# Performance work log

Measured on AMD Instinct MI355X. Metric: run time of the kernel, lower is better.

## Reference

```python
import jax, jax.numpy as jnp
import numpy as np

# --- static module config (from init_kwargs) ---
C1_OUT = 64          # c1OutChannels
C1K = 400            # k winners in conv layer
N_FC = 1024          # fc1 hidden units (n)
K_FC = 100           # k winners in fc1
BOOST = 1.0          # boostStrength
W_SPARSITY = 0.5     # weightSparsity: fraction of fc1 weights allowed nonzero
HP = 12              # pooled spatial size: floor((28-5+1)/2)
C1_OUTPUT_LEN = C1_OUT * HP * HP  # 9216
BATCH = 4096


def setup_inputs() -> dict:
    key = jax.random.key(0)
    ks = jax.random.split(key, 10)
    x = jax.random.normal(ks[0], (BATCH, 1, 28, 28), jnp.float32)
    c1_w = jax.random.normal(ks[1], (C1_OUT, 1, 5, 5), jnp.float32) * 0.1
    c1_b = jax.random.normal(ks[2], (C1_OUT,), jnp.float32) * 0.01
    # duty cycles live in [0, ~density]
    duty_cnn = jax.random.uniform(ks[3], (1, C1_OUT, 1, 1), jnp.float32) * 0.05
    fc1_w = jax.random.normal(ks[4], (N_FC, C1_OUT_LEN_ := C1_OUTPUT_LEN), jnp.float32) * 0.01
    fc1_mask_raw = jax.random.uniform(ks[5], (N_FC, C1_OUTPUT_LEN), jnp.float32)
    fc1_b = jax.random.normal(ks[6], (N_FC,), jnp.float32) * 0.01
    duty_fc = jax.random.uniform(ks[7], (N_FC,), jnp.float32) * 0.1
    fc2_w = jax.random.normal(ks[8], (10, N_FC), jnp.float32) * 0.05
    fc2_b = jnp.zeros((10,), jnp.float32)
    return dict(x=x, c1_w=c1_w, c1_b=c1_b, duty_cnn=duty_cnn, fc1_w=fc1_w,
                fc1_mask_raw=fc1_mask_raw, fc1_b=fc1_b, duty_fc=duty_fc,
                fc2_w=fc2_w, fc2_b=fc2_b)


def _kwinners(x_flat, boost_flat, k):
    """Duty-cycle-boosted k-winner mask.
    x_flat: [B, N]; boost_flat: [1, N] broadcastable boost factors.
    Keeps original x values at the top-k boosted positions per row, zeros rest.
    Boosting uses stop_gradient(x), matching KWinners*.forward(x.detach()*boost).
    """
    boosted = jax.lax.stop_gradient(x_flat) * boost_flat
    thr = jax.lax.top_k(boosted, k)[0][:, -1:]  # k-th largest per row
    return jnp.where(boosted >= thr, x_flat, jnp.zeros((), x_flat.dtype))


def reference(x, c1_w, c1_b, duty_cnn, fc1_w, fc1_mask_raw, fc1_b, duty_fc,
              fc2_w, fc2_b):
    B = x.shape[0]
    # conv2d (valid, stride 1) -> [B, 64, 24, 24]
    y = jax.lax.conv_general_dilated(
        x, c1_w, window_strides=(1, 1), padding='VALID',
        dimension_numbers=('NCHW', 'OIHW', 'NCHW')) + c1_b[None, :, None, None]
    # max_pool2d(2) -> [B, 64, 12, 12]
    y = jax.lax.reduce_window(y, -jnp.inf, jax.lax.max,
                              (1, 1, 2, 2), (1, 1, 2, 2), 'VALID')
    # KWinnersCNN: global top-k over flattened (C,H,W), per-channel boost
    target_density = C1K / C1_OUTPUT_LEN
    boost_c = jnp.exp((target_density - duty_cnn) * BOOST)  # [1,C,1,1]
    boost_flat = jnp.broadcast_to(boost_c, (1, C1_OUT, HP, HP)).reshape(1, -1)
    yf = _kwinners(y.reshape(B, -1), boost_flat, C1K)  # [B, 9216]
    # LinearSDR fc1: sparse-weight linear + KWinners
    w_mask = (fc1_mask_raw < W_SPARSITY).astype(fc1_w.dtype)
    h = yf @ (fc1_w * w_mask).T + fc1_b  # [B, 1024]
    boost_fc = jnp.exp((K_FC / N_FC - duty_fc) * BOOST)[None, :]
    h = _kwinners(h, boost_fc, K_FC)
    # fc2 + log_softmax (dropout inactive in eval mode)
    logits = h @ fc2_w.T + fc2_b
    return jax.nn.log_softmax(logits, axis=1)
```

## Files before the change

kernel.cpp:

```cpp
#include <hip/hip_runtime.h>

__device__ __forceinline__ float b2f(unsigned short u) {
  return __uint_as_float(((unsigned)u) << 16);
}
__device__ __forceinline__ unsigned short f2b(float f) {
  unsigned u = __float_as_uint(f);
  return (unsigned short)((u + 0x7FFFu + ((u >> 16) & 1u)) >> 16);
}
__device__ __forceinline__ float gload(const void* p, int i, int isb) {
  return isb ? b2f(((const unsigned short*)p)[i]) : ((const float*)p)[i];
}
__device__ __forceinline__ unsigned tokey(float f) {
  unsigned u = __float_as_uint(f);
  return u ^ (unsigned)(((int)u >> 31) | 0x80000000u);
}

__global__ void k_detect(const void* x, int* flag) {
  int tid = threadIdx.x;
  unsigned short u = ((const unsigned short*)x)[2 * tid];
  int e = (u >> 7) & 0xFF;
  bool sane = (e >= 100 && e <= 140);
  unsigned long long m = __ballot(sane);
  if (tid == 0) *flag = (__popcll(m) >= 40) ? 1 : 0;
}

__global__ __launch_bounds__(256) void k_prep(const void* __restrict__ fc1w,
                                              const void* __restrict__ mraw,
                                              float* __restrict__ WtF,
                                              const int* __restrict__ flag) {
  __shared__ float tile[64][65];
  const int isb = *flag;
  const int i0 = blockIdx.x * 64;
  const int u0 = blockIdx.y * 64;
  const int tx = threadIdx.x & 63, ty = threadIdx.x >> 6;
  for (int uu = ty; uu < 64; uu += 4) {
    int gi = (u0 + uu) * 9216 + i0 + tx;
    float wv = gload(fc1w, gi, isb);
    float mv = gload(mraw, gi, isb);
    tile[uu][tx] = (mv < 0.5f) ? wv : 0.0f;
  }
  __syncthreads();
  for (int ii = ty; ii < 64; ii += 4)
    WtF[(i0 + ii) * 1024 + u0 + tx] = tile[tx][ii];
}

__global__ __launch_bounds__(256) void k_conv(const void* __restrict__ x,
                                              const void* __restrict__ c1w_g,
                                              const void* __restrict__ c1b_g,
                                              const void* __restrict__ duty_g,
                                              int2* __restrict__ wpair,
                                              int* __restrict__ wcnt,
                                              const int* __restrict__ flag) {
  __shared__ __align__(16) unsigned char u_imghist[3136];
  __shared__ float cb[64], bcs[64];
  __shared__ __align__(16) float pooled[9216];
  __shared__ unsigned wtot[4];
  __shared__ unsigned selb, selk;
  float* img = (float*)u_imghist;
  unsigned* h2a = (unsigned*)u_imghist;
  unsigned* h2b = (unsigned*)(u_imghist + 1024);
  const int tid = threadIdx.x;
  const int b = blockIdx.x;
  const int isb = *flag;
  const int lane = tid & 63;
  const int wv_id = tid >> 6;

  for (int i = tid; i < 784; i += 256) img[i] = gload(x, b * 784 + i, isb);
  if (tid < 64) {
    cb[tid] = gload(c1b_g, tid, isb);
    float arg = (float)(400.0 / 9216.0) - gload(duty_g, tid, isb);
    bcs[tid] = (float)exp((double)arg);
  }
  __syncthreads();

  {
    const int c = tid >> 2;
    const int half = tid & 1;
    const int ph0 = ((tid >> 1) & 1) * 6;
    float w[25];
#pragma unroll
    for (int i = 0; i < 25; ++i) w[i] = gload(c1w_g, c * 25 + i, isb);
    const float bias = cb[c];
    float R[6][16];
#pragma unroll
    for (int r = 0; r < 6; ++r) {
      int ir = 2 * ph0 + r;
#pragma unroll
      for (int q = 0; q < 4; ++q)
        ((float4*)&R[r][0])[q] = ((const float4*)img)[ir * 7 + half * 3 + q];
    }
#pragma unroll
    for (int i = 0; i < 6; ++i) {
      const int ph = ph0 + i;
      float a0[12], a1[12];
#pragma unroll
      for (int j = 0; j < 12; ++j) { a0[j] = 0.f; a1[j] = 0.f; }
#pragma unroll
      for (int kj = 0; kj < 5; ++kj) {
#pragma unroll
        for (int kr = 0; kr < 5; ++kr) {
          float wk = w[kr * 5 + kj];
          const float* r0 = &R[(2 * i + kr) % 6][0];
          const float* r1 = &R[(2 * i + kr + 1) % 6][0];
#pragma unroll
          for (int j = 0; j < 12; ++j) {
            a0[j] = fmaf(r0[j + kj], wk, a0[j]);
            a1[j] = fmaf(r1[j + kj], wk, a1[j]);
          }
        }
      }
      int obase = c * 144 + ph * 12 + half * 6;
#pragma unroll
      for (int q = 0; q < 6; ++q) {
        float m = fmaxf(fmaxf(a0[2 * q], a0[2 * q + 1]),
                        fmaxf(a1[2 * q], a1[2 * q + 1]));
        pooled[obase + q] = m + bias;
      }
      if (i < 5) {
        int ir0 = 2 * ph + 6, ir1 = 2 * ph + 7;
        float* d0 = &R[(2 * i) % 6][0];
        float* d1 = &R[(2 * i + 1) % 6][0];
#pragma unroll
        for (int q = 0; q < 4; ++q) {
          ((float4*)d0)[q] = ((const float4*)img)[ir0 * 7 + half * 3 + q];
          ((float4*)d1)[q] = ((const float4*)img)[ir1 * 7 + half * 3 + q];
        }
      }
    }
  }
  __syncthreads();

  unsigned keys[36];
  {
    const float bcf = bcs[tid >> 2];
#pragma unroll
    for (int e4 = 0; e4 < 9; ++e4) {
      float4 pv = ((float4*)pooled)[tid * 9 + e4];
      keys[4 * e4 + 0] = tokey(pv.x * bcf);
      keys[4 * e4 + 1] = tokey(pv.y * bcf);
      keys[4 * e4 + 2] = tokey(pv.z * bcf);
      keys[4 * e4 + 3] = tokey(pv.w * bcf);
    }
  }

  unsigned kfix = 0;
  unsigned kk = 400;
  for (int pass = 3; pass >= 0; --pass) {
    const int shift = pass * 8;
    const unsigned himask = (pass == 3) ? 0u : (0xFFFFFFFFu << (shift + 8));
    h2a[tid] = 0;
    h2b[tid] = 0;
    __syncthreads();
    unsigned* myh = (wv_id < 2) ? h2a : h2b;
    if (pass == 3) {
      unsigned cbin = keys[0] >> 24, ccnt = 1;
#pragma unroll
      for (int e = 1; e < 36; ++e) {
        unsigned bin = keys[e] >> 24;
        if (bin == cbin) {
          ++ccnt;
        } else {
          atomicAdd(&myh[cbin], ccnt);
          cbin = bin;
          ccnt = 1;
        }
      }
      atomicAdd(&myh[cbin], ccnt);
    } else {
#pragma unroll
      for (int e = 0; e < 36; ++e) {
        unsigned key = keys[e];
        if (((key ^ kfix) & himask) == 0)
          atomicAdd(&myh[(key >> shift) & 255u], 1u);
      }
    }
    __syncthreads();
    unsigned own = h2a[tid] + h2b[tid];
    unsigned v = own;
#pragma unroll
    for (int off = 1; off < 64; off <<= 1) {
      unsigned y = __shfl_down(v, off, 64);
      if (lane + off < 64) v += y;
    }
    if (lane == 0) wtot[wv_id] = v;
    __syncthreads();
#pragma unroll
    for (int w2 = 0; w2 < 4; ++w2)
      if (w2 > wv_id) v += wtot[w2];
    unsigned snext = v - own;
    if (v >= kk && snext < kk) {
      selb = (unsigned)tid;
      selk = kk - snext;
    }
    __syncthreads();
    kfix |= selb << shift;
    kk = selk;
  }

  unsigned mycnt = 0;
#pragma unroll
  for (int e = 0; e < 36; ++e) mycnt += (keys[e] >= kfix) ? 1u : 0u;
  unsigned px = mycnt;
#pragma unroll
  for (int off = 1; off < 64; off <<= 1) {
    unsigned y = __shfl_up(px, off, 64);
    if (lane >= off) px += y;
  }
  if (lane == 63) wtot[wv_id] = px;
  __syncthreads();
  unsigned base = 0;
#pragma unroll
  for (int w2 = 0; w2 < 4; ++w2)
    if (w2 < wv_id) base += wtot[w2];
  int pos = (int)(base + px - mycnt);
  for (int e = 0; e < 36; ++e) {
    if (keys[e] >= kfix) {
      int o = tid * 36 + e;
      if (pos < 512)
        wpair[b * 512 + pos] = make_int2(__float_as_int(pooled[o]), o << 12);
      ++pos;
    }
  }
  if (tid == 0) {
    unsigned tot = wtot[0] + wtot[1] + wtot[2] + wtot[3];
    wcnt[b] = (int)(tot < 512u ? tot : 512u);
  }
}

__global__ __launch_bounds__(128) void k_fc1(const float* __restrict__ WtF,
                                             const int2* __restrict__ wpair,
                                             const int* __restrict__ wcnt,
                                             const void* __restrict__ fc1b,
                                             float* __restrict__ h,
                                             const int* __restrict__ flag) {
  __shared__ __align__(16) int2 wl[512];
  const int tid = threadIdx.x;
  const int img = blockIdx.x >> 3;
  const int slice = blockIdx.x & 7;
  const int isb = *flag;
  const int cnt = wcnt[img];
  const int2* __restrict__ wp = wpair + img * 512;
  for (int i = tid; i < cnt; i += 128) wl[i] = wp[i];
  __syncthreads();
  const int u = (slice << 7) + tid;
  const char* __restrict__ Wb = (const char*)WtF + (unsigned)u * 4u;
  const int4* wl4 = (const int4*)wl;
  float acc = 0.f;
  int w = 0;
  for (; w + 8 <= cnt; w += 8) {
    const int b4 = w >> 1;
    int4 q0 = wl4[b4 + 0];
    int4 q1 = wl4[b4 + 1];
    int4 q2 = wl4[b4 + 2];
    int4 q3 = wl4[b4 + 3];
    acc = fmaf(__int_as_float(q0.x), *(const float*)(Wb + (unsigned)q0.y), acc);
    acc = fmaf(__int_as_float(q0.z), *(const float*)(Wb + (unsigned)q0.w), acc);
    acc = fmaf(__int_as_float(q1.x), *(const float*)(Wb + (unsigned)q1.y), acc);
    acc = fmaf(__int_as_float(q1.z), *(const float*)(Wb + (unsigned)q1.w), acc);
    acc = fmaf(__int_as_float(q2.x), *(const float*)(Wb + (unsigned)q2.y), acc);
    acc = fmaf(__int_as_float(q2.z), *(const float*)(Wb + (unsigned)q2.w), acc);
    acc = fmaf(__int_as_float(q3.x), *(const float*)(Wb + (unsigned)q3.y), acc);
    acc = fmaf(__int_as_float(q3.z), *(const float*)(Wb + (unsigned)q3.w), acc);
  }
  for (; w < cnt; ++w) {
    int2 p = wl[w];
    acc = fmaf(__int_as_float(p.x), *(const float*)(Wb + (unsigned)p.y), acc);
  }
  h[img * 1024 + u] = acc + gload(fc1b, u, isb);
}

__global__ __launch_bounds__(256) void k_boost(const void* __restrict__ dutyfc,
                                               float* __restrict__ bf,
                                               const int* __restrict__ flag) {
  const int u = blockIdx.x * 256 + threadIdx.x;
  const int isb = *flag;
  if (u < 1024)
    bf[u] = (float)exp((double)(0.09765625f - gload(dutyfc, u, isb)));
}

__global__ __launch_bounds__(256) void k_sel(const float* __restrict__ h,
                                             const float* __restrict__ bf,
                                             const void* __restrict__ fc2w,
                                             const void* __restrict__ fc2b,
                                             void* __restrict__ out,
                                             const int* __restrict__ flag) {
  __shared__ __align__(16) unsigned whist[4][256];
  const int tid = threadIdx.x;
  const int lane = tid & 63;
  const int wv = tid >> 6;
  const int row = blockIdx.x * 4 + wv;
  const int isb = *flag;
  unsigned* hist = whist[wv];
  volatile unsigned* vhist = whist[wv];

  float hv[16];
  unsigned keys[16];
#pragma unroll
  for (int j = 0; j < 16; ++j) {
    float xv = h[row * 1024 + j * 64 + lane];
    hv[j] = xv;
    keys[j] = tokey(xv * bf[j * 64 + lane]);
  }

  unsigned kfix = 0, kk = 100;
  for (int pass = 3; pass >= 0; --pass) {
    const int shift = pass * 8;
    const unsigned himask = (pass == 3) ? 0u : (0xFFFFFFFFu << (shift + 8));
    ((uint4*)hist)[lane] = make_uint4(0u, 0u, 0u, 0u);
    __builtin_amdgcn_sched_barrier(0);
#pragma unroll
    for (int j = 0; j < 16; ++j) {
      if (((keys[j] ^ kfix) & himask) == 0)
        atomicAdd(&hist[(keys[j] >> shift) & 255u], 1u);
    }
    __builtin_amdgcn_sched_barrier(0);
    unsigned o0 = vhist[4 * lane + 0];
    unsigned o1 = vhist[4 * lane + 1];
    unsigned o2 = vhist[4 * lane + 2];
    unsigned o3 = vhist[4 * lane + 3];
    unsigned lsum = o0 + o1 + o2 + o3;
    unsigned v = lsum;
#pragma unroll
    for (int off = 1; off < 64; off <<= 1) {
      unsigned y = __shfl_down(v, off, 64);
      if (lane + off < 64) v += y;
    }
    const unsigned after = v - lsum;
    const unsigned t3 = o3;
    const unsigned t2 = o2 + t3;
    const unsigned t1 = o1 + t2;
    const unsigned t0 = o0 + t1;
    unsigned candb = 0, candk = 0;
    bool found = false;
    const unsigned S0 = after + t0, S1 = after + t1, S2 = after + t2,
                   S3 = after + t3, S4 = after;
    if (S0 >= kk && S1 < kk) { candb = 4u * lane + 0u; candk = kk - S1; found = true; }
    else if (S1 >= kk && S2 < kk) { candb = 4u * lane + 1u; candk = kk - S2; found = true; }
    else if (S2 >= kk && S3 < kk) { candb = 4u * lane + 2u; candk = kk - S3; found = true; }
    else if (S3 >= kk && S4 < kk) { candb = 4u * lane + 3u; candk = kk - S4; found = true; }
    unsigned long long msk = __ballot(found);
    int src = __ffsll((unsigned long long)msk) - 1;
    candb = __shfl(candb, src, 64);
    candk = __shfl(candk, src, 64);
    kfix |= candb << shift;
    kk = candk;
  }

  double part[10];
#pragma unroll
  for (int c = 0; c < 10; ++c) part[c] = 0.0;
#pragma unroll
  for (int j = 0; j < 16; ++j) {
    if (keys[j] >= kfix) {
      const int u = j * 64 + lane;
      const double hx = (double)hv[j];
#pragma unroll
      for (int c = 0; c < 10; ++c)
        part[c] = fma(hx, (double)gload(fc2w, c * 1024 + u, isb), part[c]);
    }
  }
#pragma unroll
  for (int c = 0; c < 10; ++c) {
    double p = part[c];
#pragma unroll
    for (int off = 32; off > 0; off >>= 1) p += __shfl_xor(p, off);
    part[c] = p + (double)gload(fc2b, c, isb);
  }

  double m = part[0];
#pragma unroll
  for (int c = 1; c < 10; ++c) m = part[c] > m ? part[c] : m;
  double mv = part[0];
#pragma unroll
  for (int c = 1; c < 10; ++c)
    if (lane == c) mv = part[c];
  double e = (lane < 10) ? exp(mv - m) : 0.0;
  double sum = 0.0;
#pragma unroll
  for (int c = 0; c < 10; ++c) sum += __shfl(e, c, 64);
  double logs = log(sum);
  if (lane < 10) {
    double o = mv - m - logs;
    if (isb)
      ((unsigned short*)out)[row * 10 + lane] = f2b((float)o);
    else
      ((float*)out)[row * 10 + lane] = (float)o;
  }
}

extern "C" void kernel_launch(void* const* d_in, const int* in_sizes, int n_in,
                              void* d_out, int out_size, void* d_ws, size_t ws_size,
                              hipStream_t stream) {
  char* ws = (char*)d_ws;
  float* WtF = (float*)ws;
  int2* wpair = (int2*)(ws + 37748736);
  int* wcnt = (int*)(ws + 54525952);
  float* h = (float*)(ws + 54542336);
  int* flag = (int*)(ws + 71319552);
  float* bf = WtF;

  k_detect<<<1, 64, 0, stream>>>(d_in[0], flag);
  k_prep<<<dim3(144, 16), 256, 0, stream>>>(d_in[4], d_in[5], WtF, flag);
  k_conv<<<4096, 256, 0, stream>>>(d_in[0], d_in[1], d_in[2], d_in[3],
                                   wpair, wcnt, flag);
  k_fc1<<<4096 * 8, 128, 0, stream>>>(WtF, wpair, wcnt, d_in[6], h, flag);
  k_boost<<<4, 256, 0, stream>>>(d_in[7], bf, flag);
  k_sel<<<1024, 256, 0, stream>>>(h, bf, d_in[8], d_in[9], d_out, flag);
}
```

Before: 564.7 us.

## Split fc1 gather into two passes over halves of the feature index range

```diff
diff --git a/kernel.cpp b/kernel.cpp
--- a/kernel.cpp
+++ b/kernel.cpp
@@ -232,7 +232,8 @@
                                              const int* __restrict__ wcnt,
                                              const void* __restrict__ fc1b,
                                              float* __restrict__ h,
-                                             const int* __restrict__ flag) {
+                                             const int* __restrict__ flag,
+                                             int phase) {
   __shared__ __align__(16) int2 wl[512];
   const int tid = threadIdx.x;
   const int img = blockIdx.x >> 3;
@@ -242,12 +243,26 @@
   const int2* __restrict__ wp = wpair + img * 512;
   for (int i = tid; i < cnt; i += 128) wl[i] = wp[i];
   __syncthreads();
+  const int CUTY = 4608 << 12;
+  int lo = 0, hi = cnt;
+  while (lo < hi) {
+    int mid = (lo + hi) >> 1;
+    if (wl[mid].y < CUTY) lo = mid + 1; else hi = mid;
+  }
+  const int cut = lo;
   const int u = (slice << 7) + tid;
   const char* __restrict__ Wb = (const char*)WtF + (unsigned)u * 4u;
   const int4* wl4 = (const int4*)wl;
-  float acc = 0.f;
-  int w = 0;
-  for (; w + 8 <= cnt; w += 8) {
+  const int wbeg = phase ? cut : 0;
+  const int wend = phase ? cnt : cut;
+  float acc = phase ? h[img * 1024 + u] : 0.f;
+  int w = wbeg;
+  if ((w & 1) && w < wend) {
+    int2 p = wl[w];
+    acc = fmaf(__int_as_float(p.x), *(const float*)(Wb + (unsigned)p.y), acc);
+    ++w;
+  }
+  for (; w + 8 <= wend; w += 8) {
     const int b4 = w >> 1;
     int4 q0 = wl4[b4 + 0];
     int4 q1 = wl4[b4 + 1];
@@ -262,11 +277,14 @@
     acc = fmaf(__int_as_float(q3.x), *(const float*)(Wb + (unsigned)q3.y), acc);
     acc = fmaf(__int_as_float(q3.z), *(const float*)(Wb + (unsigned)q3.w), acc);
   }
-  for (; w < cnt; ++w) {
+  for (; w < wend; ++w) {
     int2 p = wl[w];
     acc = fmaf(__int_as_float(p.x), *(const float*)(Wb + (unsigned)p.y), acc);
   }
-  h[img * 1024 + u] = acc + gload(fc1b, u, isb);
+  if (phase)
+    h[img * 1024 + u] = acc + gload(fc1b, u, isb);
+  else
+    h[img * 1024 + u] = acc;
 }
 
 __global__ __launch_bounds__(256) void k_boost(const void* __restrict__ dutyfc,
@@ -403,7 +421,8 @@
   k_prep<<<dim3(144, 16), 256, 0, stream>>>(d_in[4], d_in[5], WtF, flag);
   k_conv<<<4096, 256, 0, stream>>>(d_in[0], d_in[1], d_in[2], d_in[3],
                                    wpair, wcnt, flag);
-  k_fc1<<<4096 * 8, 128, 0, stream>>>(WtF, wpair, wcnt, d_in[6], h, flag);
+  k_fc1<<<4096 * 8, 128, 0, stream>>>(WtF, wpair, wcnt, d_in[6], h, flag, 0);
+  k_fc1<<<4096 * 8, 128, 0, stream>>>(WtF, wpair, wcnt, d_in[6], h, flag, 1);
   k_boost<<<4, 256, 0, stream>>>(d_in[7], bf, flag);
   k_sel<<<1024, 256, 0, stream>>>(h, bf, d_in[8], d_in[9], d_out, flag);
 }
```

Measured after the change: 555.9 us. Within noise of the previous version (-1.6%).

## Split fc1 gather into two phases by index range and inline dtype detection

Applied to the files above, without the earlier changes.

```diff
diff --git a/kernel.cpp b/kernel.cpp
--- a/kernel.cpp
+++ b/kernel.cpp
@@ -14,22 +14,26 @@
   unsigned u = __float_as_uint(f);
   return u ^ (unsigned)(((int)u >> 31) | 0x80000000u);
 }
-
-__global__ void k_detect(const void* x, int* flag) {
-  int tid = threadIdx.x;
+__device__ __forceinline__ int detect_isb_wave0(const void* x, int tid) {
   unsigned short u = ((const unsigned short*)x)[2 * tid];
   int e = (u >> 7) & 0xFF;
-  bool sane = (e >= 100 && e <= 140);
-  unsigned long long m = __ballot(sane);
-  if (tid == 0) *flag = (__popcll(m) >= 40) ? 1 : 0;
-}
-
-__global__ __launch_bounds__(256) void k_prep(const void* __restrict__ fc1w,
+  unsigned long long m = __ballot(e >= 100 && e <= 140);
+  return (__popcll(m) >= 40) ? 1 : 0;
+}
+
+__global__ __launch_bounds__(256) void k_prep(const void* __restrict__ x,
+                                              const void* __restrict__ fc1w,
                                               const void* __restrict__ mraw,
-                                              float* __restrict__ WtF,
-                                              const int* __restrict__ flag) {
+                                              float* __restrict__ WtF) {
   __shared__ float tile[64][65];
-  const int isb = *flag;
+  __shared__ int sflag;
+  const int tid = threadIdx.x;
+  if (tid < 64) {
+    int f = detect_isb_wave0(x, tid);
+    if (tid == 0) sflag = f;
+  }
+  __syncthreads();
+  const int isb = sflag;
   const int i0 = blockIdx.x * 64;
   const int u0 = blockIdx.y * 64;
   const int tx = threadIdx.x & 63, ty = threadIdx.x >> 6;
@@ -49,21 +53,27 @@
                                               const void* __restrict__ c1b_g,
                                               const void* __restrict__ duty_g,
                                               int2* __restrict__ wpair,
-                                              int* __restrict__ wcnt,
-                                              const int* __restrict__ flag) {
+                                              int* __restrict__ wcnt) {
   __shared__ __align__(16) unsigned char u_imghist[3136];
   __shared__ float cb[64], bcs[64];
   __shared__ __align__(16) float pooled[9216];
   __shared__ unsigned wtot[4];
   __shared__ unsigned selb, selk;
+  __shared__ int sflag;
   float* img = (float*)u_imghist;
   unsigned* h2a = (unsigned*)u_imghist;
   unsigned* h2b = (unsigned*)(u_imghist + 1024);
   const int tid = threadIdx.x;
   const int b = blockIdx.x;
-  const int isb = *flag;
   const int lane = tid & 63;
   const int wv_id = tid >> 6;
+
+  if (tid < 64) {
+    int f = detect_isb_wave0(x, tid);
+    if (tid == 0) sflag = f;
+  }
+  __syncthreads();
+  const int isb = sflag;
 
   for (int i = tid; i < 784; i += 256) img[i] = gload(x, b * 784 + i, isb);
   if (tid < 64) {
@@ -223,7 +233,10 @@
   }
   if (tid == 0) {
     unsigned tot = wtot[0] + wtot[1] + wtot[2] + wtot[3];
-    wcnt[b] = (int)(tot < 512u ? tot : 512u);
+    unsigned cut = wtot[0] + wtot[1];
+    if (tot > 512u) tot = 512u;
+    if (cut > 512u) cut = 512u;
+    wcnt[b] = (int)(tot | (cut << 16));
   }
 }
 
@@ -232,22 +245,32 @@
                                              const int* __restrict__ wcnt,
                                              const void* __restrict__ fc1b,
                                              float* __restrict__ h,
-                                             const int* __restrict__ flag) {
+                                             const void* __restrict__ x,
+                                             int phase) {
   __shared__ __align__(16) int2 wl[512];
+  __shared__ int sflag;
   const int tid = threadIdx.x;
   const int img = blockIdx.x >> 3;
   const int slice = blockIdx.x & 7;
-  const int isb = *flag;
-  const int cnt = wcnt[img];
-  const int2* __restrict__ wp = wpair + img * 512;
-  for (int i = tid; i < cnt; i += 128) wl[i] = wp[i];
-  __syncthreads();
+  if (tid < 64) {
+    int f = detect_isb_wave0(x, tid);
+    if (tid == 0) sflag = f;
+  }
+  const unsigned wc = (unsigned)wcnt[img];
+  const int cnt = (int)(wc & 0xFFFFu);
+  const int cut = (int)(wc >> 16);
+  const int beg = phase ? cut : 0;
+  const int len = (phase ? cnt : cut) - beg;
+  const int2* __restrict__ wp = wpair + img * 512 + beg;
+  for (int i = tid; i < len; i += 128) wl[i] = wp[i];
+  __syncthreads();
+  const int isb = sflag;
   const int u = (slice << 7) + tid;
   const char* __restrict__ Wb = (const char*)WtF + (unsigned)u * 4u;
   const int4* wl4 = (const int4*)wl;
-  float acc = 0.f;
+  float acc = phase ? h[img * 1024 + u] : 0.f;
   int w = 0;
-  for (; w + 8 <= cnt; w += 8) {
+  for (; w + 8 <= len; w += 8) {
     const int b4 = w >> 1;
     int4 q0 = wl4[b4 + 0];
     int4 q1 = wl4[b4 + 1];
@@ -262,34 +285,38 @@
     acc = fmaf(__int_as_float(q3.x), *(const float*)(Wb + (unsigned)q3.y), acc);
     acc = fmaf(__int_as_float(q3.z), *(const float*)(Wb + (unsigned)q3.w), acc);
   }
-  for (; w < cnt; ++w) {
+  for (; w < len; ++w) {
     int2 p = wl[w];
     acc = fmaf(__int_as_float(p.x), *(const float*)(Wb + (unsigned)p.y), acc);
   }
-  h[img * 1024 + u] = acc + gload(fc1b, u, isb);
-}
-
-__global__ __launch_bounds__(256) void k_boost(const void* __restrict__ dutyfc,
-                                               float* __restrict__ bf,
-                                               const int* __restrict__ flag) {
-  const int u = blockIdx.x * 256 + threadIdx.x;
-  const int isb = *flag;
-  if (u < 1024)
-    bf[u] = (float)exp((double)(0.09765625f - gload(dutyfc, u, isb)));
+  if (phase)
+    h[img * 1024 + u] = acc + gload(fc1b, u, isb);
+  else
+    h[img * 1024 + u] = acc;
 }
 
 __global__ __launch_bounds__(256) void k_sel(const float* __restrict__ h,
-                                             const float* __restrict__ bf,
+                                             const void* __restrict__ dutyfc,
                                              const void* __restrict__ fc2w,
                                              const void* __restrict__ fc2b,
                                              void* __restrict__ out,
-                                             const int* __restrict__ flag) {
+                                             const void* __restrict__ x) {
   __shared__ __align__(16) unsigned whist[4][256];
+  __shared__ __align__(16) float bfl[1024];
+  __shared__ int sflag;
   const int tid = threadIdx.x;
   const int lane = tid & 63;
   const int wv = tid >> 6;
   const int row = blockIdx.x * 4 + wv;
-  const int isb = *flag;
+  if (tid < 64) {
+    int f = detect_isb_wave0(x, tid);
+    if (tid == 0) sflag = f;
+  }
+  __syncthreads();
+  const int isb = sflag;
+  for (int i = tid; i < 1024; i += 256)
+    bfl[i] = (float)exp((double)(0.09765625f - gload(dutyfc, i, isb)));
+  __syncthreads();
   unsigned* hist = whist[wv];
   volatile unsigned* vhist = whist[wv];
 
@@ -299,7 +326,7 @@
   for (int j = 0; j < 16; ++j) {
     float xv = h[row * 1024 + j * 64 + lane];
     hv[j] = xv;
-    keys[j] = tokey(xv * bf[j * 64 + lane]);
+    keys[j] = tokey(xv * bfl[j * 64 + lane]);
   }
 
   unsigned kfix = 0, kk = 100;
@@ -396,14 +423,11 @@
   int2* wpair = (int2*)(ws + 37748736);
   int* wcnt = (int*)(ws + 54525952);
   float* h = (float*)(ws + 54542336);
-  int* flag = (int*)(ws + 71319552);
-  float* bf = WtF;
-
-  k_detect<<<1, 64, 0, stream>>>(d_in[0], flag);
-  k_prep<<<dim3(144, 16), 256, 0, stream>>>(d_in[4], d_in[5], WtF, flag);
+
+  k_prep<<<dim3(144, 16), 256, 0, stream>>>(d_in[0], d_in[4], d_in[5], WtF);
   k_conv<<<4096, 256, 0, stream>>>(d_in[0], d_in[1], d_in[2], d_in[3],
-                                   wpair, wcnt, flag);
-  k_fc1<<<4096 * 8, 128, 0, stream>>>(WtF, wpair, wcnt, d_in[6], h, flag);
-  k_boost<<<4, 256, 0, stream>>>(d_in[7], bf, flag);
-  k_sel<<<1024, 256, 0, stream>>>(h, bf, d_in[8], d_in[9], d_out, flag);
-}
+                                   wpair, wcnt);
+  k_fc1<<<4096 * 8, 128, 0, stream>>>(WtF, wpair, wcnt, d_in[6], h, d_in[0], 0);
+  k_fc1<<<4096 * 8, 128, 0, stream>>>(WtF, wpair, wcnt, d_in[6], h, d_in[0], 1);
+  k_sel<<<1024, 256, 0, stream>>>(h, d_in[7], d_in[8], d_in[9], d_out, d_in[0]);
+}
```

Result: faster. 545.5 us (-3.4%).

## Split fc1 gather into two feature-range phases and fold boost into selection

Applied to the files above, without the earlier changes.

```diff
diff --git a/kernel.cpp b/kernel.cpp
--- a/kernel.cpp
+++ b/kernel.cpp
@@ -223,7 +223,10 @@
   }
   if (tid == 0) {
     unsigned tot = wtot[0] + wtot[1] + wtot[2] + wtot[3];
-    wcnt[b] = (int)(tot < 512u ? tot : 512u);
+    unsigned cut = wtot[0] + wtot[1];
+    if (tot > 512u) tot = 512u;
+    if (cut > 512u) cut = 512u;
+    wcnt[b] = (int)(tot | (cut << 16));
   }
 }
 
@@ -232,22 +235,27 @@
                                              const int* __restrict__ wcnt,
                                              const void* __restrict__ fc1b,
                                              float* __restrict__ h,
-                                             const int* __restrict__ flag) {
+                                             const int* __restrict__ flag,
+                                             int phase) {
   __shared__ __align__(16) int2 wl[512];
   const int tid = threadIdx.x;
   const int img = blockIdx.x >> 3;
   const int slice = blockIdx.x & 7;
   const int isb = *flag;
-  const int cnt = wcnt[img];
-  const int2* __restrict__ wp = wpair + img * 512;
-  for (int i = tid; i < cnt; i += 128) wl[i] = wp[i];
+  const unsigned wc = (unsigned)wcnt[img];
+  const int cnt = (int)(wc & 0xFFFFu);
+  const int cut = (int)(wc >> 16);
+  const int beg = phase ? cut : 0;
+  const int len = (phase ? cnt : cut) - beg;
+  const int2* __restrict__ wp = wpair + img * 512 + beg;
+  for (int i = tid; i < len; i += 128) wl[i] = wp[i];
   __syncthreads();
   const int u = (slice << 7) + tid;
   const char* __restrict__ Wb = (const char*)WtF + (unsigned)u * 4u;
   const int4* wl4 = (const int4*)wl;
-  float acc = 0.f;
+  float acc = phase ? h[img * 1024 + u] : 0.f;
   int w = 0;
-  for (; w + 8 <= cnt; w += 8) {
+  for (; w + 8 <= len; w += 8) {
     const int b4 = w >> 1;
     int4 q0 = wl4[b4 + 0];
     int4 q1 = wl4[b4 + 1];
@@ -262,34 +270,32 @@
     acc = fmaf(__int_as_float(q3.x), *(const float*)(Wb + (unsigned)q3.y), acc);
     acc = fmaf(__int_as_float(q3.z), *(const float*)(Wb + (unsigned)q3.w), acc);
   }
-  for (; w < cnt; ++w) {
+  for (; w < len; ++w) {
     int2 p = wl[w];
     acc = fmaf(__int_as_float(p.x), *(const float*)(Wb + (unsigned)p.y), acc);
   }
-  h[img * 1024 + u] = acc + gload(fc1b, u, isb);
-}
-
-__global__ __launch_bounds__(256) void k_boost(const void* __restrict__ dutyfc,
-                                               float* __restrict__ bf,
-                                               const int* __restrict__ flag) {
-  const int u = blockIdx.x * 256 + threadIdx.x;
-  const int isb = *flag;
-  if (u < 1024)
-    bf[u] = (float)exp((double)(0.09765625f - gload(dutyfc, u, isb)));
+  if (phase)
+    h[img * 1024 + u] = acc + gload(fc1b, u, isb);
+  else
+    h[img * 1024 + u] = acc;
 }
 
 __global__ __launch_bounds__(256) void k_sel(const float* __restrict__ h,
-                                             const float* __restrict__ bf,
+                                             const void* __restrict__ dutyfc,
                                              const void* __restrict__ fc2w,
                                              const void* __restrict__ fc2b,
                                              void* __restrict__ out,
                                              const int* __restrict__ flag) {
   __shared__ __align__(16) unsigned whist[4][256];
+  __shared__ __align__(16) float bfl[1024];
   const int tid = threadIdx.x;
   const int lane = tid & 63;
   const int wv = tid >> 6;
   const int row = blockIdx.x * 4 + wv;
   const int isb = *flag;
+  for (int i = tid; i < 1024; i += 256)
+    bfl[i] = (float)exp((double)(0.09765625f - gload(dutyfc, i, isb)));
+  __syncthreads();
   unsigned* hist = whist[wv];
   volatile unsigned* vhist = whist[wv];
 
@@ -299,7 +305,7 @@
   for (int j = 0; j < 16; ++j) {
     float xv = h[row * 1024 + j * 64 + lane];
     hv[j] = xv;
-    keys[j] = tokey(xv * bf[j * 64 + lane]);
+    keys[j] = tokey(xv * bfl[j * 64 + lane]);
   }
 
   unsigned kfix = 0, kk = 100;
@@ -397,13 +403,12 @@
   int* wcnt = (int*)(ws + 54525952);
   float* h = (float*)(ws + 54542336);
   int* flag = (int*)(ws + 71319552);
-  float* bf = WtF;
 
   k_detect<<<1, 64, 0, stream>>>(d_in[0], flag);
   k_prep<<<dim3(144, 16), 256, 0, stream>>>(d_in[4], d_in[5], WtF, flag);
   k_conv<<<4096, 256, 0, stream>>>(d_in[0], d_in[1], d_in[2], d_in[3],
                                    wpair, wcnt, flag);
-  k_fc1<<<4096 * 8, 128, 0, stream>>>(WtF, wpair, wcnt, d_in[6], h, flag);
-  k_boost<<<4, 256, 0, stream>>>(d_in[7], bf, flag);
-  k_sel<<<1024, 256, 0, stream>>>(h, bf, d_in[8], d_in[9], d_out, flag);
-}
+  k_fc1<<<4096 * 8, 128, 0, stream>>>(WtF, wpair, wcnt, d_in[6], h, flag, 0);
+  k_fc1<<<4096 * 8, 128, 0, stream>>>(WtF, wpair, wcnt, d_in[6], h, flag, 1);
+  k_sel<<<1024, 256, 0, stream>>>(h, d_in[7], d_in[8], d_in[9], d_out, flag);
+}
```

Measured after the change: 540.3 us. 1.05x faster.
